# Kernel tuning notes

Measured on AMD Instinct MI355X. Metric: run time of the kernel, lower is better.

Reference implementation:

```python
import jax, jax.numpy as jnp
import numpy as np

B, T, H, L, V, NL = 32, 512, 1024, 2, 32000, 5
PAD = 0


def setup_inputs() -> dict:
    key = jax.random.key(0)
    ks = jax.random.split(key, 8)
    s = 0.02
    emb = jax.random.normal(ks[2], (V, H), jnp.float32) * s
    emb = emb.at[PAD].set(0.0)  # mimic padding_idx init
    return {
        "x": jax.random.randint(ks[0], (B, T), 0, V),
        "labels": jax.random.randint(ks[1], (B,), 0, NL),
        "emb": emb,
        "W_ih": jax.random.normal(ks[3], (L, 4 * H, H), jnp.float32) * s,
        "W_hh": jax.random.normal(ks[4], (L, 4 * H, H), jnp.float32) * s,
        "b": jnp.zeros((L, 4 * H), jnp.float32),
        "fc_W": jax.random.normal(ks[5], (NL, H), jnp.float32) * s,
        "fc_b": jnp.zeros((NL,), jnp.float32),
    }


def _lstm_layer(seq, Wih, Whh, b):
    # seq: [T, B, H] time-major; standard LSTM, PyTorch gate order i,f,g,o
    h_dim = Whh.shape[-1]
    bsz = seq.shape[1]
    h0 = jnp.zeros((bsz, h_dim), seq.dtype)
    c0 = jnp.zeros((bsz, h_dim), seq.dtype)

    def step(carry, x_t):
        h, c = carry
        g = x_t @ Wih.T + h @ Whh.T + b  # [B, 4H]
        i, f, gg, o = jnp.split(g, 4, axis=-1)
        c = jax.nn.sigmoid(f) * c + jax.nn.sigmoid(i) * jnp.tanh(gg)
        h = jax.nn.sigmoid(o) * jnp.tanh(c)
        return (h, c), h

    _, hs = jax.lax.scan(step, (h0, c0), seq)
    return hs  # [T, B, H]


def reference(x, labels, emb, W_ih, W_hh, b, fc_W, fc_b):
    # embed then go time-major: [B,T] -> [T,B,H]
    seq = jnp.transpose(emb[x], (1, 0, 2))
    for l in range(W_ih.shape[0]):
        seq = _lstm_layer(seq, W_ih[l], W_hh[l], b[l])
    logits = seq[-1] @ fc_W.T + fc_b  # [B, NL]
    logp = jax.nn.log_softmax(logits, axis=-1)
    loss = -jnp.mean(jnp.take_along_axis(logp, labels[:, None], axis=1))
    return (loss, logits)
```

## Files before the change

kernel.cpp:

```cpp
#include <hip/hip_runtime.h>

typedef unsigned short u16;
typedef unsigned int   u32;
typedef unsigned long long u64;
typedef __attribute__((ext_vector_type(8))) short short8;
typedef __attribute__((ext_vector_type(4))) float f32x4;
typedef __attribute__((ext_vector_type(16))) float f32x16;

#define OFF_H1   134217728ull
#define OFF_H2   (OFF_H1 + 131072ull)
#define OFF_H2F  (OFF_H2 + 131072ull)
#define OFF_CNT  (OFF_H2F + 131072ull)

__device__ inline u16 f2bf(float f) {
  u32 x = __float_as_uint(f);
  x += 0x7fffu + ((x >> 16) & 1u);
  return (u16)(x >> 16);
}
__device__ inline float bf2f(u16 u) { return __uint_as_float(((u32)u) << 16); }

__device__ inline short8 pack_bf16x8(float4 a, float4 b) {
  short8 r;
  r[0] = (short)f2bf(a.x); r[1] = (short)f2bf(a.y); r[2] = (short)f2bf(a.z); r[3] = (short)f2bf(a.w);
  r[4] = (short)f2bf(b.x); r[5] = (short)f2bf(b.y); r[6] = (short)f2bf(b.z); r[7] = (short)f2bf(b.w);
  return r;
}

__device__ inline f32x16 mfma32(short8 a, short8 b, f32x16 c) {
  return __builtin_amdgcn_mfma_f32_32x32x16_bf16(a, b, c, 0, 0, 0);
}

__device__ inline float sigf(float x) { return 1.f / (1.f + __expf(-x)); }
__device__ inline float tanhfast(float x) {
  x = fminf(15.f, fmaxf(-15.f, x));
  float e = __expf(2.f * x);
  return (e - 1.f) / (e + 1.f);
}

__device__ inline void load16_frags(const char* a0, uint4 f[16]) {
  const char* a1 = a0 + 4096;
  const char* a2 = a0 + 8192;
  const char* a3 = a0 + 12288;
  asm volatile(
    "global_load_dwordx4 %0, %16, off sc0 sc1\n\t"
    "global_load_dwordx4 %1, %16, off offset:1024 sc0 sc1\n\t"
    "global_load_dwordx4 %2, %16, off offset:2048 sc0 sc1\n\t"
    "global_load_dwordx4 %3, %16, off offset:3072 sc0 sc1\n\t"
    "global_load_dwordx4 %4, %17, off sc0 sc1\n\t"
    "global_load_dwordx4 %5, %17, off offset:1024 sc0 sc1\n\t"
    "global_load_dwordx4 %6, %17, off offset:2048 sc0 sc1\n\t"
    "global_load_dwordx4 %7, %17, off offset:3072 sc0 sc1\n\t"
    "global_load_dwordx4 %8, %18, off sc0 sc1\n\t"
    "global_load_dwordx4 %9, %18, off offset:1024 sc0 sc1\n\t"
    "global_load_dwordx4 %10, %18, off offset:2048 sc0 sc1\n\t"
    "global_load_dwordx4 %11, %18, off offset:3072 sc0 sc1\n\t"
    "global_load_dwordx4 %12, %19, off sc0 sc1\n\t"
    "global_load_dwordx4 %13, %19, off offset:1024 sc0 sc1\n\t"
    "global_load_dwordx4 %14, %19, off offset:2048 sc0 sc1\n\t"
    "global_load_dwordx4 %15, %19, off offset:3072 sc0 sc1\n\t"
    "s_waitcnt vmcnt(0)"
    : "=&v"(f[0]), "=&v"(f[1]), "=&v"(f[2]), "=&v"(f[3]),
      "=&v"(f[4]), "=&v"(f[5]), "=&v"(f[6]), "=&v"(f[7]),
      "=&v"(f[8]), "=&v"(f[9]), "=&v"(f[10]), "=&v"(f[11]),
      "=&v"(f[12]), "=&v"(f[13]), "=&v"(f[14]), "=&v"(f[15])
    : "v"(a0), "v"(a1), "v"(a2), "v"(a3));
}

__global__ void init_zero_k(uint4* __restrict__ z, int n4, u32* __restrict__ cnt) {
  const int i = blockIdx.x * blockDim.x + threadIdx.x;
  if (i < n4)  z[i] = make_uint4(0u, 0u, 0u, 0u);
  if (i < 256) cnt[i] = 0u;
}

__global__ __launch_bounds__(256) void gemm_g1(
    const int* __restrict__ x, const float* __restrict__ emb,
    const float* __restrict__ Wih, u16* __restrict__ G1)
{
  __shared__ __align__(16) u16 lsbuf[2 * 128 * 72];
  __shared__ int tokoff[128];
  u16* lA = lsbuf;
  u16* lB = lsbuf + 128 * 72;
  u16* ltile = lsbuf;

  const int tid = threadIdx.x;
  const int ntb = blockIdx.x & 31;
  const int mtb = blockIdx.x >> 5;

  if (tid < 128) {
    const int n = mtb * 128 + tid;
    tokoff[tid] = x[(n & 31) * 512 + (n >> 5)];
  }
  __syncthreads();

  const int lane = tid & 63;
  const int wv = tid >> 6;
  const int wm = (wv & 1) * 64;
  const int wn = (wv >> 1) * 64;

  const f32x4 zero = {0.f, 0.f, 0.f, 0.f};
  f32x4 acc[4][4];
#pragma unroll
  for (int i = 0; i < 4; ++i)
#pragma unroll
    for (int j = 0; j < 4; ++j) acc[i][j] = zero;

  const int rowS = tid >> 1;
  const int kh = (tid & 1) * 32;
  const size_t embrow = (size_t)tokoff[rowS] * 1024;
  const size_t wihrow = (size_t)(ntb * 128 + rowS) * 1024;

  for (int kk = 0; kk < 1024; kk += 64) {
    __syncthreads();
    {
      const float4* sa = (const float4*)(emb + embrow + kk + kh);
      const float4* sb = (const float4*)(Wih + wihrow + kk + kh);
#pragma unroll
      for (int v = 0; v < 4; ++v) {
        *(short8*)&lA[rowS * 72 + kh + v * 8] = pack_bf16x8(sa[2 * v], sa[2 * v + 1]);
        *(short8*)&lB[rowS * 72 + kh + v * 8] = pack_bf16x8(sb[2 * v], sb[2 * v + 1]);
      }
    }
    __syncthreads();
#pragma unroll
    for (int ks = 0; ks < 2; ++ks) {
      short8 aF[4], bF[4];
#pragma unroll
      for (int i = 0; i < 4; ++i)
        aF[i] = *(const short8*)&lA[(wm + i * 16 + (lane & 15)) * 72 + ks * 32 + (lane >> 4) * 8];
#pragma unroll
      for (int i = 0; i < 4; ++i)
        bF[i] = *(const short8*)&lB[(wn + i * 16 + (lane & 15)) * 72 + ks * 32 + (lane >> 4) * 8];
#pragma unroll
      for (int i = 0; i < 4; ++i)
#pragma unroll
        for (int j = 0; j < 4; ++j)
          acc[i][j] = __builtin_amdgcn_mfma_f32_16x16x32_bf16(aF[i], bF[j], acc[i][j], 0, 0, 0);
    }
  }
  __syncthreads();

#pragma unroll
  for (int i = 0; i < 4; ++i)
#pragma unroll
    for (int j = 0; j < 4; ++j)
#pragma unroll
      for (int r = 0; r < 4; ++r)
        ltile[(wm + i * 16 + (lane >> 4) * 4 + r) * 136 + wn + j * 16 + (lane & 15)] =
            f2bf(acc[i][j][r]);
  __syncthreads();

  const int gate = ntb >> 3;
  const int w0 = (ntb & 7) * 16;
  const int chunkid = tid >> 2;
  const int part = tid & 3;
  const int tloc = chunkid >> 4;
  const int wloc = chunkid & 15;
  const size_t base =
      ((size_t)((mtb * 4 + tloc) * 128 + w0 + wloc) * 4 + gate) * 256;
#pragma unroll
  for (int m = 0; m < 8; ++m) {
    const int idx = part * 64 + m * 8;
    const int u = idx >> 5;
    const int b0 = idx & 31;
    union { u16 h[8]; uint4 q; } t;
#pragma unroll
    for (int k = 0; k < 8; ++k)
      t.h[k] = ltile[(tloc * 32 + b0 + k) * 136 + wloc * 8 + u];
    *(uint4*)(G1 + base + idx) = t.q;
  }
}

__device__ inline void gbar(u32* cnt, u32 target) {
  asm volatile("" ::: "memory");
  if (threadIdx.x == 0)
    __hip_atomic_fetch_add(cnt + ((blockIdx.x & 7) << 5), 1u,
                           __ATOMIC_RELAXED, __HIP_MEMORY_SCOPE_AGENT);
  if (threadIdx.x < 64) {
    int guard = 0;
    for (;;) {
      u32 v = 0;
      if (threadIdx.x < 8)
        v = __hip_atomic_load(cnt + (threadIdx.x << 5),
                              __ATOMIC_RELAXED, __HIP_MEMORY_SCOPE_AGENT);
      v += __shfl_xor(v, 1);
      v += __shfl_xor(v, 2);
      v += __shfl_xor(v, 4);
      v = __shfl(v, 0);
      if (v >= target) break;
      if (++guard > (1 << 20)) break;
      __builtin_amdgcn_s_sleep(1);
    }
  }
  __syncthreads();
  asm volatile("" ::: "memory");
}

__global__ __launch_bounds__(256, 1) void lstm_recur(
    const float* __restrict__ Wih_all, const float* __restrict__ Whh_all,
    const float* __restrict__ bias_all, const u16* __restrict__ G1,
    u64* __restrict__ h1buf, u64* __restrict__ h2buf,
    float* __restrict__ h2f, u32* __restrict__ cnt)
{
  __shared__ float gp[4][32][33];
  __shared__ __align__(16) u16 hpack[32 * 8];

  const int tid = threadIdx.x;
  const int lane = tid & 63;
  const int wv = tid >> 6;
  const int bid = blockIdx.x;
  const int layer = bid >> 7;
  const int w = bid & 127;

  const int pu = tid & 7;
  const int pb = tid >> 3;
  float creg = 0.f;
  float bs0, bs1, bs2, bs3;
  {
    const float* bb = bias_all + layer * 4096 + w * 8 + pu;
    bs0 = bb[0]; bs1 = bb[1024]; bs2 = bb[2048]; bs3 = bb[3072];
  }

  const int K0w = (layer == 0) ? (wv * 256) : ((wv & 1) * 512);
  const int nA = lane & 31;
  const int kpart = (lane >> 5) * 8;
  const size_t wrow = (size_t)((nA >> 3) * 1024 + w * 8 + (nA & 7)) * 1024;
  const float* Wsrc = (layer == 0) ? Whh_all
                    : ((wv < 2) ? (Wih_all + 4194304) : (Whh_all + 4194304));

  short8 bw[32];
#pragma unroll
  for (int ks = 0; ks < 16; ++ks) {
    const float* p = Wsrc + wrow + (K0w + ks * 16 + kpart);
    bw[ks] = pack_bf16x8(((const float4*)p)[0], ((const float4*)p)[1]);
  }
  if (layer == 1) {
#pragma unroll
    for (int ks = 16; ks < 32; ++ks) {
      const float* p = Wsrc + wrow + (K0w + ks * 16 + kpart);
      bw[ks] = pack_bf16x8(((const float4*)p)[0], ((const float4*)p)[1]);
    }
  }

  const int aoff = (((K0w >> 3) + (lane >> 5)) * 32 + (lane & 31)) * 16;

  float g0 = 0.f, g1v = 0.f, g2 = 0.f, g3 = 0.f;
  if (layer == 0) {
    const u16* gpt = G1 + (size_t)w * 1024 + pu * 32 + pb;
    g0 = bf2f(gpt[0]); g1v = bf2f(gpt[256]); g2 = bf2f(gpt[512]); g3 = bf2f(gpt[768]);
  }

  for (int s = 0; s <= 512; ++s) {
    const bool active = (layer == 0) ? (s < 512) : (s >= 1);
    if (active) {
      const char* hb;
      if (layer == 0) {
        hb = (const char*)(h1buf + (size_t)((s - 1) & 1) * 8192);
      } else {
        const int t2 = s - 1;
        hb = (wv < 2) ? (const char*)(h1buf + (size_t)(t2 & 1) * 8192)
                      : (const char*)(h2buf + (size_t)((t2 - 1) & 1) * 8192);
      }
      const char* a0 = hb + aoff;
      f32x16 acc = {0.f,0.f,0.f,0.f,0.f,0.f,0.f,0.f,0.f,0.f,0.f,0.f,0.f,0.f,0.f,0.f};
      uint4 f[16];
      load16_frags(a0, f);
      if (layer == 0) {
#pragma unroll
        for (int i = 0; i < 16; ++i)
          acc = mfma32(__builtin_bit_cast(short8, f[i]), bw[i], acc);
      } else {
#pragma unroll
        for (int i = 0; i < 16; ++i)
          acc = mfma32(__builtin_bit_cast(short8, f[i]), bw[i], acc);
        load16_frags(a0 + 16384, f);
#pragma unroll
        for (int i = 0; i < 16; ++i)
          acc = mfma32(__builtin_bit_cast(short8, f[i]), bw[16 + i], acc);
      }
#pragma unroll
      for (int r = 0; r < 16; ++r)
        gp[wv][(r & 3) + 8 * (r >> 2) + 4 * (lane >> 5)][lane & 31] = acc[r];
    }
    __syncthreads();
    if (active) {
      float gi = bs0 + g0, gf = bs1 + g1v, gg = bs2 + g2, go = bs3 + g3;
#pragma unroll
      for (int q = 0; q < 4; ++q) {
        gi += gp[q][pb][pu];
        gf += gp[q][pb][8 + pu];
        gg += gp[q][pb][16 + pu];
        go += gp[q][pb][24 + pu];
      }
      creg = sigf(gf) * creg + sigf(gi) * tanhfast(gg);
      const float hval = sigf(go) * tanhfast(creg);
      hpack[pb * 8 + pu] = f2bf(hval);
      if (layer == 1 && s == 512) h2f[pb * 1024 + w * 8 + pu] = hval;
    }
    __syncthreads();
    if (active && s < 512 && tid < 32) {
      const u64* hp = (const u64*)(hpack + tid * 8);
      const u64 lo = hp[0], hi = hp[1];
      u64* dst = (layer == 0) ? (h1buf + (size_t)(s & 1) * 8192)
                              : (h2buf + (size_t)((s - 1) & 1) * 8192);
      const int chunk = w * 32 + tid;
      __hip_atomic_store(dst + chunk * 2,     lo, __ATOMIC_RELAXED, __HIP_MEMORY_SCOPE_AGENT);
      __hip_atomic_store(dst + chunk * 2 + 1, hi, __ATOMIC_RELAXED, __HIP_MEMORY_SCOPE_AGENT);
    }
    if (layer == 0 && s + 1 < 512) {
      const u16* gpt = G1 + ((size_t)(s + 1) * 128 + w) * 1024 + pu * 32 + pb;
      g0 = bf2f(gpt[0]); g1v = bf2f(gpt[256]); g2 = bf2f(gpt[512]); g3 = bf2f(gpt[768]);
    }
    if (s < 512) {
      if (wv == 0) __builtin_amdgcn_s_waitcnt(0);
      gbar(cnt, 256u * (u32)(s + 1));
    }
  }
}

__global__ __launch_bounds__(256) void epilogue_k(
    const float* __restrict__ h2f, const float* __restrict__ fcW,
    const float* __restrict__ fcb, const int* __restrict__ labels,
    float* __restrict__ out)
{
  __shared__ float slog[160];
  __shared__ float snll[32];
  const int tid = threadIdx.x;
  const int lane = tid & 63;
  const int wv = tid >> 6;
  for (int d = wv * 40; d < (wv + 1) * 40; ++d) {
    const int b = d / 5, l = d - b * 5;
    const float* hr = h2f + b * 1024 + lane * 16;
    const float* wr = fcW + l * 1024 + lane * 16;
    float sacc = 0.f;
#pragma unroll
    for (int i = 0; i < 16; ++i) sacc += hr[i] * wr[i];
#pragma unroll
    for (int off = 32; off > 0; off >>= 1) sacc += __shfl_down(sacc, off);
    if (lane == 0) slog[d] = sacc + fcb[l];
  }
  __syncthreads();
  if (tid < 32) {
    const int b = tid;
    float m = slog[b * 5];
    for (int l = 1; l < 5; ++l) m = fmaxf(m, slog[b * 5 + l]);
    float se = 0.f;
    for (int l = 0; l < 5; ++l) se += __expf(slog[b * 5 + l] - m);
    const float lse = m + __logf(se);
    for (int l = 0; l < 5; ++l) out[1 + b * 5 + l] = slog[b * 5 + l];
    snll[b] = lse - slog[b * 5 + labels[b]];
  }
  __syncthreads();
  if (tid == 0) {
    float a = 0.f;
    for (int b = 0; b < 32; ++b) a += snll[b];
    out[0] = a * (1.f / 32.f);
  }
}

extern "C" void kernel_launch(void* const* d_in, const int* in_sizes, int n_in,
                              void* d_out, int out_size, void* d_ws, size_t ws_size,
                              hipStream_t stream)
{
  const int*   x      = (const int*)  d_in[0];
  const int*   labels = (const int*)  d_in[1];
  const float* emb    = (const float*)d_in[2];
  const float* W_ih   = (const float*)d_in[3];
  const float* W_hh   = (const float*)d_in[4];
  const float* bias   = (const float*)d_in[5];
  const float* fcW    = (const float*)d_in[6];
  const float* fcb    = (const float*)d_in[7];
  float* out = (float*)d_out;

  char* ws = (char*)d_ws;
  u16* G1    = (u16*)ws;
  u64* h1buf = (u64*)(ws + OFF_H1);
  u64* h2buf = (u64*)(ws + OFF_H2);
  float* h2f = (float*)(ws + OFF_H2F);
  u32* cnt   = (u32*)(ws + OFF_CNT);

  init_zero_k<<<dim3(64), dim3(256), 0, stream>>>((uint4*)(ws + OFF_H1), 16384, cnt);
  gemm_g1<<<dim3(4096), dim3(256), 0, stream>>>(x, emb, W_ih, G1);
  lstm_recur<<<dim3(256), dim3(256), 0, stream>>>(W_ih, W_hh, bias, G1, h1buf, h2buf, h2f, cnt);
  epilogue_k<<<dim3(1), dim3(256), 0, stream>>>(h2f, fcW, fcb, labels, out);
}
```

Measured before the change: 3.903 ms.

## Replace global barrier with per-layer counters, ring buffer, and 512-thread blocks

Swaps the single grid-wide barrier for separate per-layer progress counters, so layer 0 can run up to three steps ahead of layer 1 through a 4-slot h1 ring buffer. Layer 1 now waits only on layer 0's current step and its own previous step. Each block doubles to 8 waves, halving per-wave K work and the weight registers each wave holds, and layer 1 uses two independent accumulators. This aims to cut barrier stalls and per-step latency, at the cost of more LDS reduction traffic and more complex synchronisation logic.

```diff
diff --git a/kernel.cpp b/kernel.cpp
--- a/kernel.cpp
+++ b/kernel.cpp
@@ -8,7 +8,7 @@
 typedef __attribute__((ext_vector_type(16))) float f32x16;
 
 #define OFF_H1   134217728ull
-#define OFF_H2   (OFF_H1 + 131072ull)
+#define OFF_H2   (OFF_H1 + 262144ull)
 #define OFF_H2F  (OFF_H2 + 131072ull)
 #define OFF_CNT  (OFF_H2F + 131072ull)
 
@@ -37,10 +37,27 @@
   return (e - 1.f) / (e + 1.f);
 }
 
-__device__ inline void load16_frags(const char* a0, uint4 f[16]) {
+__device__ inline void load8_frags(const char* a0, uint4 f[8]) {
   const char* a1 = a0 + 4096;
-  const char* a2 = a0 + 8192;
-  const char* a3 = a0 + 12288;
+  asm volatile(
+    "global_load_dwordx4 %0, %8, off sc0 sc1\n\t"
+    "global_load_dwordx4 %1, %8, off offset:1024 sc0 sc1\n\t"
+    "global_load_dwordx4 %2, %8, off offset:2048 sc0 sc1\n\t"
+    "global_load_dwordx4 %3, %8, off offset:3072 sc0 sc1\n\t"
+    "global_load_dwordx4 %4, %9, off sc0 sc1\n\t"
+    "global_load_dwordx4 %5, %9, off offset:1024 sc0 sc1\n\t"
+    "global_load_dwordx4 %6, %9, off offset:2048 sc0 sc1\n\t"
+    "global_load_dwordx4 %7, %9, off offset:3072 sc0 sc1\n\t"
+    "s_waitcnt vmcnt(0)"
+    : "=&v"(f[0]), "=&v"(f[1]), "=&v"(f[2]), "=&v"(f[3]),
+      "=&v"(f[4]), "=&v"(f[5]), "=&v"(f[6]), "=&v"(f[7])
+    : "v"(a0), "v"(a1));
+}
+
+__device__ inline void load16_dual(const char* aI, const char* aH,
+                                   uint4 fI[8], uint4 fH[8]) {
+  const char* aI1 = aI + 4096;
+  const char* aH1 = aH + 4096;
   asm volatile(
     "global_load_dwordx4 %0, %16, off sc0 sc1\n\t"
     "global_load_dwordx4 %1, %16, off offset:1024 sc0 sc1\n\t"
@@ -59,17 +76,17 @@
     "global_load_dwordx4 %14, %19, off offset:2048 sc0 sc1\n\t"
     "global_load_dwordx4 %15, %19, off offset:3072 sc0 sc1\n\t"
     "s_waitcnt vmcnt(0)"
-    : "=&v"(f[0]), "=&v"(f[1]), "=&v"(f[2]), "=&v"(f[3]),
-      "=&v"(f[4]), "=&v"(f[5]), "=&v"(f[6]), "=&v"(f[7]),
-      "=&v"(f[8]), "=&v"(f[9]), "=&v"(f[10]), "=&v"(f[11]),
-      "=&v"(f[12]), "=&v"(f[13]), "=&v"(f[14]), "=&v"(f[15])
-    : "v"(a0), "v"(a1), "v"(a2), "v"(a3));
+    : "=&v"(fI[0]), "=&v"(fI[1]), "=&v"(fI[2]), "=&v"(fI[3]),
+      "=&v"(fI[4]), "=&v"(fI[5]), "=&v"(fI[6]), "=&v"(fI[7]),
+      "=&v"(fH[0]), "=&v"(fH[1]), "=&v"(fH[2]), "=&v"(fH[3]),
+      "=&v"(fH[4]), "=&v"(fH[5]), "=&v"(fH[6]), "=&v"(fH[7])
+    : "v"(aI), "v"(aI1), "v"(aH), "v"(aH1));
 }
 
 __global__ void init_zero_k(uint4* __restrict__ z, int n4, u32* __restrict__ cnt) {
   const int i = blockIdx.x * blockDim.x + threadIdx.x;
-  if (i < n4)  z[i] = make_uint4(0u, 0u, 0u, 0u);
-  if (i < 256) cnt[i] = 0u;
+  if (i < n4)   z[i] = make_uint4(0u, 0u, 0u, 0u);
+  if (i < 2048) cnt[i] = 0u;
 }
 
 __global__ __launch_bounds__(256) void gemm_g1(
@@ -170,23 +187,23 @@
   }
 }
 
-__device__ inline void gbar(u32* cnt, u32 target) {
-  asm volatile("" ::: "memory");
-  if (threadIdx.x == 0)
-    __hip_atomic_fetch_add(cnt + ((blockIdx.x & 7) << 5), 1u,
-                           __ATOMIC_RELAXED, __HIP_MEMORY_SCOPE_AGENT);
-  if (threadIdx.x < 64) {
+__device__ inline void gwait(u32* cnt, int t0, int t1) {
+  if (threadIdx.x < 64 && (t0 > 0 || t1 > 0)) {
     int guard = 0;
     for (;;) {
-      u32 v = 0;
+      int v = 0;
       if (threadIdx.x < 8)
-        v = __hip_atomic_load(cnt + (threadIdx.x << 5),
-                              __ATOMIC_RELAXED, __HIP_MEMORY_SCOPE_AGENT);
+        v = (int)__hip_atomic_load(cnt + threadIdx.x * 32,
+                                   __ATOMIC_RELAXED, __HIP_MEMORY_SCOPE_AGENT);
+      else if (threadIdx.x < 16)
+        v = (int)__hip_atomic_load(cnt + 1024 + (threadIdx.x - 8) * 32,
+                                   __ATOMIC_RELAXED, __HIP_MEMORY_SCOPE_AGENT);
       v += __shfl_xor(v, 1);
       v += __shfl_xor(v, 2);
       v += __shfl_xor(v, 4);
-      v = __shfl(v, 0);
-      if (v >= target) break;
+      const int s0 = __shfl(v, 0);
+      const int s1 = __shfl(v, 8);
+      if (s0 >= t0 && s1 >= t1) break;
       if (++guard > (1 << 20)) break;
       __builtin_amdgcn_s_sleep(1);
     }
@@ -195,13 +212,13 @@
   asm volatile("" ::: "memory");
 }
 
-__global__ __launch_bounds__(256, 1) void lstm_recur(
+__global__ __launch_bounds__(512, 2) void lstm_recur(
     const float* __restrict__ Wih_all, const float* __restrict__ Whh_all,
     const float* __restrict__ bias_all, const u16* __restrict__ G1,
-    u64* __restrict__ h1buf, u64* __restrict__ h2buf,
+    u64* __restrict__ h1ring, u64* __restrict__ h2buf,
     float* __restrict__ h2f, u32* __restrict__ cnt)
 {
-  __shared__ float gp[4][32][33];
+  __shared__ float gp[8][32][33];
   __shared__ __align__(16) u16 hpack[32 * 8];
 
   const int tid = threadIdx.x;
@@ -211,81 +228,80 @@
   const int layer = bid >> 7;
   const int w = bid & 127;
 
-  const int pu = tid & 7;
-  const int pb = tid >> 3;
+  const int pu = (tid >> 5) & 7;
+  const int pb = tid & 31;
+  const bool pw_act = tid < 256;
   float creg = 0.f;
-  float bs0, bs1, bs2, bs3;
-  {
+  float bs0 = 0.f, bs1 = 0.f, bs2 = 0.f, bs3 = 0.f;
+  if (pw_act) {
     const float* bb = bias_all + layer * 4096 + w * 8 + pu;
     bs0 = bb[0]; bs1 = bb[1024]; bs2 = bb[2048]; bs3 = bb[3072];
   }
 
-  const int K0w = (layer == 0) ? (wv * 256) : ((wv & 1) * 512);
   const int nA = lane & 31;
   const int kpart = (lane >> 5) * 8;
   const size_t wrow = (size_t)((nA >> 3) * 1024 + w * 8 + (nA & 7)) * 1024;
-  const float* Wsrc = (layer == 0) ? Whh_all
-                    : ((wv < 2) ? (Wih_all + 4194304) : (Whh_all + 4194304));
-
-  short8 bw[32];
-#pragma unroll
-  for (int ks = 0; ks < 16; ++ks) {
-    const float* p = Wsrc + wrow + (K0w + ks * 16 + kpart);
-    bw[ks] = pack_bf16x8(((const float4*)p)[0], ((const float4*)p)[1]);
-  }
-  if (layer == 1) {
-#pragma unroll
-    for (int ks = 16; ks < 32; ++ks) {
-      const float* p = Wsrc + wrow + (K0w + ks * 16 + kpart);
-      bw[ks] = pack_bf16x8(((const float4*)p)[0], ((const float4*)p)[1]);
-    }
-  }
-
-  const int aoff = (((K0w >> 3) + (lane >> 5)) * 32 + (lane & 31)) * 16;
+  const int K0 = wv * 128;
+  short8 bw0[8], bw1[8];
+  {
+    const float* s0 = (layer == 0) ? Whh_all : (Wih_all + 4194304);
+#pragma unroll
+    for (int ks = 0; ks < 8; ++ks) {
+      const float* p = s0 + wrow + (K0 + ks * 16 + kpart);
+      bw0[ks] = pack_bf16x8(((const float4*)p)[0], ((const float4*)p)[1]);
+    }
+    if (layer == 1) {
+      const float* s1 = Whh_all + 4194304;
+#pragma unroll
+      for (int ks = 0; ks < 8; ++ks) {
+        const float* p = s1 + wrow + (K0 + ks * 16 + kpart);
+        bw1[ks] = pack_bf16x8(((const float4*)p)[0], ((const float4*)p)[1]);
+      }
+    }
+  }
+
+  const int aoff = ((wv * 16 + (lane >> 5)) * 32 + (lane & 31)) * 16;
 
   float g0 = 0.f, g1v = 0.f, g2 = 0.f, g3 = 0.f;
-  if (layer == 0) {
+  if (layer == 0 && pw_act) {
     const u16* gpt = G1 + (size_t)w * 1024 + pu * 32 + pb;
     g0 = bf2f(gpt[0]); g1v = bf2f(gpt[256]); g2 = bf2f(gpt[512]); g3 = bf2f(gpt[768]);
   }
 
-  for (int s = 0; s <= 512; ++s) {
-    const bool active = (layer == 0) ? (s < 512) : (s >= 1);
-    if (active) {
-      const char* hb;
-      if (layer == 0) {
-        hb = (const char*)(h1buf + (size_t)((s - 1) & 1) * 8192);
-      } else {
-        const int t2 = s - 1;
-        hb = (wv < 2) ? (const char*)(h1buf + (size_t)(t2 & 1) * 8192)
-                      : (const char*)(h2buf + (size_t)((t2 - 1) & 1) * 8192);
-      }
-      const char* a0 = hb + aoff;
-      f32x16 acc = {0.f,0.f,0.f,0.f,0.f,0.f,0.f,0.f,0.f,0.f,0.f,0.f,0.f,0.f,0.f,0.f};
-      uint4 f[16];
-      load16_frags(a0, f);
-      if (layer == 0) {
-#pragma unroll
-        for (int i = 0; i < 16; ++i)
-          acc = mfma32(__builtin_bit_cast(short8, f[i]), bw[i], acc);
-      } else {
-#pragma unroll
-        for (int i = 0; i < 16; ++i)
-          acc = mfma32(__builtin_bit_cast(short8, f[i]), bw[i], acc);
-        load16_frags(a0 + 16384, f);
-#pragma unroll
-        for (int i = 0; i < 16; ++i)
-          acc = mfma32(__builtin_bit_cast(short8, f[i]), bw[16 + i], acc);
-      }
-#pragma unroll
-      for (int r = 0; r < 16; ++r)
-        gp[wv][(r & 3) + 8 * (r >> 2) + 4 * (lane >> 5)][lane & 31] = acc[r];
-    }
+  for (int s = 0; s < 512; ++s) {
+    if (layer == 0) gwait(cnt, 128 * s, 128 * (s - 3));
+    else            gwait(cnt, 128 * (s + 1), 128 * s);
+
+    f32x16 accA = {0.f,0.f,0.f,0.f,0.f,0.f,0.f,0.f,0.f,0.f,0.f,0.f,0.f,0.f,0.f,0.f};
+    if (layer == 0) {
+      const char* a0 = (const char*)h1ring + (size_t)((s + 3) & 3) * 65536 + aoff;
+      uint4 f[8];
+      load8_frags(a0, f);
+#pragma unroll
+      for (int i = 0; i < 8; ++i)
+        accA = mfma32(__builtin_bit_cast(short8, f[i]), bw0[i], accA);
+    } else {
+      const char* aI = (const char*)h1ring + (size_t)(s & 3) * 65536 + aoff;
+      const char* aH = (const char*)h2buf + (size_t)((s + 1) & 1) * 65536 + aoff;
+      uint4 fI[8], fH[8];
+      load16_dual(aI, aH, fI, fH);
+      f32x16 accB = {0.f,0.f,0.f,0.f,0.f,0.f,0.f,0.f,0.f,0.f,0.f,0.f,0.f,0.f,0.f,0.f};
+#pragma unroll
+      for (int i = 0; i < 8; ++i)
+        accA = mfma32(__builtin_bit_cast(short8, fI[i]), bw0[i], accA);
+#pragma unroll
+      for (int i = 0; i < 8; ++i)
+        accB = mfma32(__builtin_bit_cast(short8, fH[i]), bw1[i], accB);
+      accA += accB;
+    }
+#pragma unroll
+    for (int r = 0; r < 16; ++r)
+      gp[wv][(r & 3) + 8 * (r >> 2) + 4 * (lane >> 5)][lane & 31] = accA[r];
     __syncthreads();
-    if (active) {
+    if (pw_act) {
       float gi = bs0 + g0, gf = bs1 + g1v, gg = bs2 + g2, go = bs3 + g3;
 #pragma unroll
-      for (int q = 0; q < 4; ++q) {
+      for (int q = 0; q < 8; ++q) {
         gi += gp[q][pb][pu];
         gf += gp[q][pb][8 + pu];
         gg += gp[q][pb][16 + pu];
@@ -294,25 +310,27 @@
       creg = sigf(gf) * creg + sigf(gi) * tanhfast(gg);
       const float hval = sigf(go) * tanhfast(creg);
       hpack[pb * 8 + pu] = f2bf(hval);
-      if (layer == 1 && s == 512) h2f[pb * 1024 + w * 8 + pu] = hval;
+      if (layer == 1 && s == 511) h2f[pb * 1024 + w * 8 + pu] = hval;
     }
     __syncthreads();
-    if (active && s < 512 && tid < 32) {
+    if (tid < 32) {
       const u64* hp = (const u64*)(hpack + tid * 8);
       const u64 lo = hp[0], hi = hp[1];
-      u64* dst = (layer == 0) ? (h1buf + (size_t)(s & 1) * 8192)
-                              : (h2buf + (size_t)((s - 1) & 1) * 8192);
+      u64* dst = (layer == 0) ? (h1ring + (size_t)(s & 3) * 8192)
+                              : (h2buf + (size_t)(s & 1) * 8192);
       const int chunk = w * 32 + tid;
       __hip_atomic_store(dst + chunk * 2,     lo, __ATOMIC_RELAXED, __HIP_MEMORY_SCOPE_AGENT);
       __hip_atomic_store(dst + chunk * 2 + 1, hi, __ATOMIC_RELAXED, __HIP_MEMORY_SCOPE_AGENT);
     }
-    if (layer == 0 && s + 1 < 512) {
+    if (wv == 0) {
+      __builtin_amdgcn_s_waitcnt(0);
+      if (tid == 0)
+        __hip_atomic_fetch_add(cnt + (layer == 0 ? 0 : 1024) + ((bid & 7) << 5), 1u,
+                               __ATOMIC_RELAXED, __HIP_MEMORY_SCOPE_AGENT);
+    }
+    if (layer == 0 && pw_act && s + 1 < 512) {
       const u16* gpt = G1 + ((size_t)(s + 1) * 128 + w) * 1024 + pu * 32 + pb;
       g0 = bf2f(gpt[0]); g1v = bf2f(gpt[256]); g2 = bf2f(gpt[512]); g3 = bf2f(gpt[768]);
-    }
-    if (s < 512) {
-      if (wv == 0) __builtin_amdgcn_s_waitcnt(0);
-      gbar(cnt, 256u * (u32)(s + 1));
     }
   }
 }
@@ -372,14 +390,14 @@
   float* out = (float*)d_out;
 
   char* ws = (char*)d_ws;
-  u16* G1    = (u16*)ws;
-  u64* h1buf = (u64*)(ws + OFF_H1);
-  u64* h2buf = (u64*)(ws + OFF_H2);
-  float* h2f = (float*)(ws + OFF_H2F);
-  u32* cnt   = (u32*)(ws + OFF_CNT);
-
-  init_zero_k<<<dim3(64), dim3(256), 0, stream>>>((uint4*)(ws + OFF_H1), 16384, cnt);
+  u16* G1     = (u16*)ws;
+  u64* h1ring = (u64*)(ws + OFF_H1);
+  u64* h2buf  = (u64*)(ws + OFF_H2);
+  float* h2f  = (float*)(ws + OFF_H2F);
+  u32* cnt    = (u32*)(ws + OFF_CNT);
+
+  init_zero_k<<<dim3(96), dim3(256), 0, stream>>>((uint4*)(ws + OFF_H1), 24576, cnt);
   gemm_g1<<<dim3(4096), dim3(256), 0, stream>>>(x, emb, W_ih, G1);
-  lstm_recur<<<dim3(256), dim3(256), 0, stream>>>(W_ih, W_hh, bias, G1, h1buf, h2buf, h2f, cnt);
+  lstm_recur<<<dim3(256), dim3(512), 0, stream>>>(W_ih, W_hh, bias, G1, h1ring, h2buf, h2f, cnt);
   epilogue_k<<<dim3(1), dim3(256), 0, stream>>>(h2f, fcW, fcb, labels, out);
 }
```

New measurement: 3.452 ms. -11.5%, faster.
